# Performance work log

Hardware: AMD Instinct MI355X
Metric: run time of the kernel (lower is better)

## Reference

```python
import jax, jax.numpy as jnp
import numpy as np

DROPOUT_P = 0.5


def normalize_adj(A):
    # A_tilda = A + I ; A_hat = D^-0.5 A_tilda D^-0.5
    # The torch code does this with diag_embed + two bmm (O(N^3));
    # mathematically it is row/col broadcasting (O(N^2)).
    B, N, _ = A.shape
    A_tilda = A + jnp.eye(N, dtype=A.dtype)
    d_inv_sqrt = jnp.sum(A_tilda, axis=2) ** -0.5          # [B, N]
    return d_inv_sqrt[:, :, None] * A_tilda * d_inv_sqrt[:, None, :]


def gcn_layer(X, A_hat, W, b):
    # standard Kipf GCN layer: A_hat @ (X @ W) + b
    return jnp.einsum('bnm,bmd->bnd', A_hat, X @ W) + b


def setup_inputs() -> dict:
    key = jax.random.key(0)
    ks = jax.random.split(key, 6)
    B, N, Din, H, C = 8, 2048, 64, 64, 16
    X = jax.random.normal(ks[0], (B, N, Din), dtype=jnp.float32)
    A = jax.random.uniform(ks[1], (B, N, N), dtype=jnp.float32)
    W1 = jax.random.normal(ks[2], (Din, H), dtype=jnp.float32) * (1.0 / np.sqrt(Din))
    b1 = jax.random.normal(ks[3], (H,), dtype=jnp.float32) * 0.01
    W2 = jax.random.normal(ks[4], (H, C), dtype=jnp.float32) * (1.0 / np.sqrt(H))
    b2 = jax.random.normal(ks[5], (C,), dtype=jnp.float32) * 0.01
    return {"X": X, "A": A, "W1": W1, "b1": b1, "W2": W2, "b2": b2}


def reference(X, A, W1, b1, W2, b2):
    A_hat = normalize_adj(A)
    h = jax.nn.relu(gcn_layer(X, A_hat, W1, b1))
    # F.dropout default training=True -> apply dropout with a fixed key
    keep = jax.random.bernoulli(jax.random.key(42), 1.0 - DROPOUT_P, h.shape)
    h = jnp.where(keep, h / (1.0 - DROPOUT_P), 0.0).astype(h.dtype)
    return gcn_layer(h, A_hat, W2, b2)
```

## Files before the change

### kernel.cpp

```cpp
#include <hip/hip_runtime.h>

#define BN 16384
#define NN 2048
#define DD 64
#define CC 16

typedef short bf16x8 __attribute__((ext_vector_type(8)));
typedef float f32x4 __attribute__((ext_vector_type(4)));
typedef unsigned short u16x4 __attribute__((ext_vector_type(4)));

__device__ __forceinline__ f32x4 mfma16(bf16x8 a, bf16x8 b, f32x4 c) {
  return __builtin_amdgcn_mfma_f32_16x16x32_bf16(a, b, c, 0, 0, 0);
}
__device__ __forceinline__ unsigned short f2bf(float f) {
  unsigned u = __float_as_uint(f);
  return (unsigned short)((u + 0x7FFFu + ((u >> 16) & 1u)) >> 16);
}
__device__ __forceinline__ float bf2f(unsigned short h) {
  return __uint_as_float(((unsigned)h) << 16);
}

__device__ __forceinline__ unsigned tf_bits(unsigned i) {
  unsigned x0 = 0u;
  unsigned x1 = i;
  const unsigned k0 = 0u, k1 = 42u, k2 = 0x1BD11BDAu ^ 0u ^ 42u;
  x0 += k0; x1 += k1;
#define TFR(r) { x0 += x1; x1 = (x1 << (r)) | (x1 >> (32 - (r))); x1 ^= x0; }
  TFR(13) TFR(15) TFR(26) TFR(6)
  x0 += k1; x1 += k2 + 1u;
  TFR(17) TFR(29) TFR(16) TFR(24)
  x0 += k2; x1 += k0 + 2u;
  TFR(13) TFR(15) TFR(26) TFR(6)
  x0 += k0; x1 += k1 + 3u;
  TFR(17) TFR(29) TFR(16) TFR(24)
  x0 += k1; x1 += k2 + 4u;
  TFR(13) TFR(15) TFR(26) TFR(6)
  x0 += k2; x1 += k0 + 5u;
#undef TFR
  return x0 ^ x1;
}


__global__ __launch_bounds__(256) void k_deg(const float* __restrict__ A,
    const float* __restrict__ X, const float* __restrict__ W1,
    float* __restrict__ dis, unsigned short* __restrict__ Abf,
    unsigned short* __restrict__ Y1s, unsigned short* __restrict__ Y1sT)
{
  const int w = threadIdx.x >> 6, lane = threadIdx.x & 63;
  const size_t row = (size_t)blockIdx.x * 4 + w;
  const float4* Arow = (const float4*)(A + row * NN);
  unsigned short* Brow = Abf + row * NN;
  float s = 0.f;
#pragma unroll
  for (int it = 0; it < 8; ++it) {
    float4 v = Arow[lane + 64 * it];
    s += (v.x + v.y) + (v.z + v.w);
    u16x4 p = { f2bf(v.x), f2bf(v.y), f2bf(v.z), f2bf(v.w) };
    *(u16x4*)(Brow + lane * 4 + it * 256) = p;
  }
#pragma unroll
  for (int m = 32; m; m >>= 1) s += __shfl_xor(s, m, 64);
  const float dv = 1.0f / sqrtf(s + 1.0f);
  if (lane == 0) dis[row] = dv;
  const float* Xr = X + row * DD;
  float acc = 0.f;
#pragma unroll
  for (int k = 0; k < DD; ++k) acc += Xr[k] * W1[k * DD + lane];
  const unsigned short yv = f2bf(dv * acc);
  Y1s[row * DD + lane] = yv;
  const int b = (int)(row >> 11), kr = (int)(row & (NN - 1));
  Y1sT[((size_t)b * DD + lane) * NN + kr] = yv;
}

__global__ __launch_bounds__(256, 4) void k_gemm1h(const unsigned short* __restrict__ Abf,
    const unsigned short* __restrict__ Y1sT, const unsigned short* __restrict__ Y1s,
    const float* __restrict__ dis, const float* __restrict__ b1,
    unsigned short* __restrict__ Hbf)
{
  __shared__ float red[4][32][36];
  const int Mb = blockIdx.x >> 1;
  const int ns = blockIdx.x & 1;
  const int w = __builtin_amdgcn_readfirstlane((int)threadIdx.x >> 6);
  const int lane = threadIdx.x & 63;
  const int m15 = lane & 15, quad = lane >> 4;
  const int b = Mb >> 6;
  const int k0 = w * 512 + quad * 8;
  const unsigned short* Ap0 = Abf + ((size_t)Mb * 32 + m15) * NN + k0;
  const unsigned short* Ap1 = Ap0 + (size_t)16 * NN;
  const unsigned short* Bp0 = Y1sT + ((size_t)b * DD + ns * 32 + m15) * NN + k0;
  const unsigned short* Bp1 = Bp0 + (size_t)16 * NN;
  const f32x4 zero = 0.f;
  f32x4 acc[2][2];
  acc[0][0] = zero; acc[0][1] = zero; acc[1][0] = zero; acc[1][1] = zero;
  bf16x8 a0 = *(const bf16x8*)Ap0, a1 = *(const bf16x8*)Ap1;
  bf16x8 b0 = *(const bf16x8*)Bp0, b1v = *(const bf16x8*)Bp1;
#pragma unroll 1
  for (int kk = 0; kk < 16; ++kk) {
    const int off = (kk < 15) ? (kk + 1) * 32 : 0;
    bf16x8 na0 = *(const bf16x8*)(Ap0 + off);
    bf16x8 na1 = *(const bf16x8*)(Ap1 + off);
    bf16x8 nb0 = *(const bf16x8*)(Bp0 + off);
    bf16x8 nb1 = *(const bf16x8*)(Bp1 + off);
    acc[0][0] = mfma16(a0, b0, acc[0][0]);
    acc[0][1] = mfma16(a0, b1v, acc[0][1]);
    acc[1][0] = mfma16(a1, b0, acc[1][0]);
    acc[1][1] = mfma16(a1, b1v, acc[1][1]);
    a0 = na0; a1 = na1; b0 = nb0; b1v = nb1;
  }
#pragma unroll
  for (int mi = 0; mi < 2; ++mi)
#pragma unroll
    for (int ni = 0; ni < 2; ++ni)
#pragma unroll
      for (int r = 0; r < 4; ++r)
        red[w][mi * 16 + quad * 4 + r][ni * 16 + m15] = acc[mi][ni][r];
  __syncthreads();
  const int tid = threadIdx.x;
  const int rowl = tid >> 3, c0 = (tid & 7) * 4;
  f32x4 sum = *(const f32x4*)&red[0][rowl][c0];
  sum += *(const f32x4*)&red[1][rowl][c0];
  sum += *(const f32x4*)&red[2][rowl][c0];
  sum += *(const f32x4*)&red[3][rowl][c0];
  const int grow = Mb * 32 + rowl;
  const int gcol0 = ns * 32 + c0;
  const u16x4 y1d = *(const u16x4*)(Y1s + (size_t)grow * DD + gcol0);
  const float4 b1q = *(const float4*)(b1 + gcol0);
  const float dv = dis[grow];
  const unsigned o0 = (unsigned)grow * DD + gcol0;
  u16x4 hq;
#pragma unroll
  for (int j = 0; j < 4; ++j) {
    const float z = sum[j] + bf2f(y1d[j]);
    const float bj = j == 0 ? b1q.x : j == 1 ? b1q.y : j == 2 ? b1q.z : b1q.w;
    float h = fmaxf(dv * z + bj, 0.f);
    const unsigned bits = tf_bits(o0 + j);
    hq[j] = (bits >> 31) ? (unsigned short)0 : f2bf(h + h);
  }
  *(u16x4*)(Hbf + (size_t)grow * DD + gcol0) = hq;
}

__global__ __launch_bounds__(256) void k_epi1(const unsigned short* __restrict__ Hbf,
    const float* __restrict__ dis, const float* __restrict__ W2,
    unsigned short* __restrict__ Y2sT, float* __restrict__ S2d)
{
  __shared__ float hs[16][68];
  __shared__ float W2l[DD * CC];
  const int tid = threadIdx.x;
  *(float4*)(W2l + tid * 4) = *(const float4*)(W2 + tid * 4);
  const int r0 = blockIdx.x * 16;
  {
    const int rl = tid >> 4, cl = (tid & 15) * 4;
    const u16x4 hv = *(const u16x4*)(Hbf + ((size_t)r0 + rl) * DD + cl);
    hs[rl][cl + 0] = bf2f(hv[0]);
    hs[rl][cl + 1] = bf2f(hv[1]);
    hs[rl][cl + 2] = bf2f(hv[2]);
    hs[rl][cl + 3] = bf2f(hv[3]);
  }
  __syncthreads();
  const int c = tid & 15, rl = tid >> 4;
  float s = 0.f;
#pragma unroll
  for (int k = 0; k < DD; ++k) s += hs[rl][k] * W2l[k * CC + c];
  const int row = r0 + rl;
  const int b = row >> 11, kr = row & (NN - 1);
  const float y2 = dis[row] * s;
  Y2sT[((size_t)b * CC + c) * NN + kr] = f2bf(y2);
  S2d[(size_t)row * CC + c] = y2;
}

__global__ __launch_bounds__(256, 4) void k_gemm2o(const unsigned short* __restrict__ Abf,
    const unsigned short* __restrict__ Y2sT, const float* __restrict__ S2d,
    const float* __restrict__ dis, const float* __restrict__ b2,
    float* __restrict__ out)
{
  __shared__ float red[4][16][20];
  const int Mb = blockIdx.x;
  const int w = __builtin_amdgcn_readfirstlane((int)threadIdx.x >> 6);
  const int lane = threadIdx.x & 63;
  const int m15 = lane & 15, quad = lane >> 4;
  const int b = Mb >> 7;
  const int k0 = w * 512 + quad * 8;
  const unsigned short* Ap = Abf + ((size_t)Mb * 16 + m15) * NN + k0;
  const unsigned short* Bp = Y2sT + ((size_t)b * CC + m15) * NN + k0;
  const f32x4 zero = 0.f;
  f32x4 acc = zero;
  bf16x8 a = *(const bf16x8*)Ap;
  bf16x8 bb = *(const bf16x8*)Bp;
#pragma unroll 1
  for (int kk = 0; kk < 16; ++kk) {
    const int off = (kk < 15) ? (kk + 1) * 32 : 0;
    bf16x8 na = *(const bf16x8*)(Ap + off);
    bf16x8 nbb = *(const bf16x8*)(Bp + off);
    acc = mfma16(a, bb, acc);
    a = na; bb = nbb;
  }
#pragma unroll
  for (int r = 0; r < 4; ++r)
    red[w][quad * 4 + r][m15] = acc[r];
  __syncthreads();
  const int tid = threadIdx.x;
  const int rowl = tid >> 4, c = tid & 15;
  const float sum = red[0][rowl][c] + red[1][rowl][c]
                  + red[2][rowl][c] + red[3][rowl][c];
  const int grow = Mb * 16 + rowl;
  out[(size_t)grow * CC + c] =
      dis[grow] * (sum + S2d[(size_t)grow * CC + c]) + b2[c];
}

#define FKS1 4
#define FKS2 16

__global__ __launch_bounds__(256) void d_deg_xw(const float* __restrict__ A,
    const float* __restrict__ X, const float* __restrict__ W1,
    float* __restrict__ dis, float* __restrict__ Y1s)
{
  const int w = threadIdx.x >> 6, lane = threadIdx.x & 63;
  const int row = __builtin_amdgcn_readfirstlane(blockIdx.x * 4 + w);
  const float4* Arow = (const float4*)(A + (size_t)row * NN);
  float s = 0.f;
#pragma unroll
  for (int it = 0; it < 8; ++it) {
    float4 v = Arow[lane + 64 * it];
    s += v.x + v.y + v.z + v.w;
  }
#pragma unroll
  for (int m = 32; m; m >>= 1) s += __shfl_xor(s, m, 64);
  const float dv = 1.0f / sqrtf(s + 1.0f);
  if (lane == 0) dis[row] = dv;
  const float* Xr = X + (size_t)row * DD;
  float acc = 0.f;
#pragma unroll
  for (int k = 0; k < DD; ++k) acc += Xr[k] * W1[k * DD + lane];
  Y1s[(size_t)row * DD + lane] = dv * acc;
}

__global__ __launch_bounds__(256) void d_gemm1(const float* __restrict__ A,
    const float* __restrict__ Y1s, float* __restrict__ Z1)
{
  const int rb = blockIdx.x >> 2, ks = blockIdx.x & (FKS1 - 1);
  const int lane = threadIdx.x & 63;
  const int c0 = __builtin_amdgcn_readfirstlane((threadIdx.x >> 6) << 4);
  const int row = rb * 64 + lane;
  const int batch = rb >> 5;
  const int KSEG = NN / FKS1;
  const float* Arow = A + (size_t)row * NN + ks * KSEG;
  const float* Yb = Y1s + (size_t)batch * NN * DD + c0;
  const int kbase = ks * KSEG;
  float acc[16];
#pragma unroll
  for (int c = 0; c < 16; ++c) acc[c] = 0.f;
  float4 a0 = *(const float4*)(Arow);
  float4 a1 = *(const float4*)(Arow + 4);
  float4 a2 = *(const float4*)(Arow + 8);
  float4 a3 = *(const float4*)(Arow + 12);
  for (int k = 0; k < KSEG; k += 16) {
    const int kn = (k + 16 < KSEG) ? (k + 16) : 0;
    float4 n0 = *(const float4*)(Arow + kn);
    float4 n1 = *(const float4*)(Arow + kn + 4);
    float4 n2 = *(const float4*)(Arow + kn + 8);
    float4 n3 = *(const float4*)(Arow + kn + 12);
    const float* y0 = Yb + (size_t)(kbase + k) * DD;
    const float av[16] = {a0.x, a0.y, a0.z, a0.w, a1.x, a1.y, a1.z, a1.w,
                          a2.x, a2.y, a2.z, a2.w, a3.x, a3.y, a3.z, a3.w};
#pragma unroll
    for (int j = 0; j < 16; ++j) {
      const float* yr = y0 + j * DD;
#pragma unroll
      for (int c = 0; c < 16; ++c) acc[c] += av[j] * yr[c];
    }
    a0 = n0; a1 = n1; a2 = n2; a3 = n3;
  }
  float* Zp = Z1 + ((size_t)ks * BN + row) * DD + c0;
#pragma unroll
  for (int c = 0; c < 16; c += 4) {
    float4 v; v.x = acc[c]; v.y = acc[c+1]; v.z = acc[c+2]; v.w = acc[c+3];
    *(float4*)(Zp + c) = v;
  }
}

__global__ __launch_bounds__(256) void d_epi1(const float* __restrict__ Z1,
    const float* __restrict__ Y1s, const float* __restrict__ dis,
    const float* __restrict__ b1, const float* __restrict__ W2,
    float* __restrict__ Y2s)
{
  __shared__ float W2l[DD * CC];
  __shared__ float hl[4][DD];
  const int tid = threadIdx.x;
  *(float4*)(W2l + tid * 4) = *(const float4*)(W2 + tid * 4);
  const int w = tid >> 6, lane = tid & 63;
  const int row = blockIdx.x * 4 + w;
  const size_t o = (size_t)row * DD + lane;
  float z = Y1s[o];
#pragma unroll
  for (int p = 0; p < FKS1; ++p) z += Z1[(size_t)p * BN * DD + o];
  const float dv = dis[row];
  float h = fmaxf(dv * z + b1[lane], 0.f);
  const unsigned bits = tf_bits((unsigned)o);
  h = (bits >> 31) ? 0.f : (h + h);
  hl[w][lane] = h;
  __syncthreads();
  const int wr = tid >> 6, l = tid & 63;
  const int c = l & 15, kq = l >> 4;
  float p = 0.f;
#pragma unroll
  for (int kk = 0; kk < 16; ++kk)
    p += hl[wr][kq * 16 + kk] * W2l[(kq * 16 + kk) * CC + c];
  p += __shfl_xor(p, 16, 64);
  p += __shfl_xor(p, 32, 64);
  if (l < 16) {
    const int rg = blockIdx.x * 4 + wr;
    Y2s[(size_t)rg * CC + c] = dis[rg] * p;
  }
}

__global__ __launch_bounds__(256) void d_gemm2(const float* __restrict__ A,
    const float* __restrict__ Y2s, float* __restrict__ Z2)
{
  const int rb = blockIdx.x >> 4, ks = blockIdx.x & (FKS2 - 1);
  const int row = rb * 256 + threadIdx.x;
  const int batch = rb >> 3;
  const int KSEG = NN / FKS2;
  const float* Arow = A + (size_t)row * NN + ks * KSEG;
  const float* Yb = Y2s + (size_t)batch * NN * CC;
  const int kbase = ks * KSEG;
  float acc[16];
#pragma unroll
  for (int c = 0; c < 16; ++c) acc[c] = 0.f;
  float4 a0 = *(const float4*)(Arow);
  float4 a1 = *(const float4*)(Arow + 4);
  for (int k = 0; k < KSEG; k += 8) {
    const int kn = (k + 8 < KSEG) ? (k + 8) : 0;
    float4 n0 = *(const float4*)(Arow + kn);
    float4 n1 = *(const float4*)(Arow + kn + 4);
    const float av[8] = {a0.x, a0.y, a0.z, a0.w, a1.x, a1.y, a1.z, a1.w};
#pragma unroll
    for (int j = 0; j < 8; ++j) {
      const float* yr = Yb + (size_t)(kbase + k + j) * CC;
#pragma unroll
      for (int c = 0; c < 16; ++c) acc[c] += av[j] * yr[c];
    }
    a0 = n0; a1 = n1;
  }
  float* Zp = Z2 + ((size_t)ks * BN + row) * CC;
#pragma unroll
  for (int c = 0; c < 16; c += 4) {
    float4 v; v.x = acc[c]; v.y = acc[c+1]; v.z = acc[c+2]; v.w = acc[c+3];
    *(float4*)(Zp + c) = v;
  }
}

__global__ __launch_bounds__(256) void d_final(const float* __restrict__ Z2,
    const float* __restrict__ Y2s, const float* __restrict__ dis,
    const float* __restrict__ b2, float* __restrict__ out)
{
  const int gid = blockIdx.x * 256 + threadIdx.x;
  const int r = gid >> 2, q = gid & 3;
  const size_t o = (size_t)r * CC + q * 4;
  float4 s = *(const float4*)(Y2s + o);
#pragma unroll
  for (int p = 0; p < FKS2; ++p) {
    const float4 zp = *(const float4*)(Z2 + (size_t)p * BN * CC + o);
    s.x += zp.x; s.y += zp.y; s.z += zp.z; s.w += zp.w;
  }
  const float dv = dis[r];
  const float4 bb = *(const float4*)(b2 + q * 4);
  float4 res;
  res.x = dv * s.x + bb.x;
  res.y = dv * s.y + bb.y;
  res.z = dv * s.z + bb.z;
  res.w = dv * s.w + bb.w;
  *(float4*)(out + o) = res;
}

extern "C" void kernel_launch(void* const* d_in, const int* in_sizes, int n_in,
                              void* d_out, int out_size, void* d_ws, size_t ws_size,
                              hipStream_t stream) {
  const float* X  = (const float*)d_in[0];
  const float* A  = (const float*)d_in[1];
  const float* W1 = (const float*)d_in[2];
  const float* b1 = (const float*)d_in[3];
  const float* W2 = (const float*)d_in[4];
  const float* b2 = (const float*)d_in[5];
  float* out = (float*)d_out;
  char* wsb = (char*)d_ws;

  const size_t NEED = 75038720;
  if (ws_size >= NEED) {
    unsigned short* Abf  = (unsigned short*)wsb;
    unsigned short* Y1s  = (unsigned short*)(wsb + 67108864);
    unsigned short* Y1sT = (unsigned short*)(wsb + 69206016);
    unsigned short* Hbf  = (unsigned short*)(wsb + 71303168);
    unsigned short* Y2sT = (unsigned short*)(wsb + 73400320);
    float*          S2d  = (float*)(wsb + 73924608);
    float*          dis  = (float*)(wsb + 74973184);

    k_deg   <<<BN / 4, 256, 0, stream>>>(A, X, W1, dis, Abf, Y1s, Y1sT);
    k_gemm1h<<<1024,   256, 0, stream>>>(Abf, Y1sT, Y1s, dis, b1, Hbf);
    k_epi1  <<<1024,   256, 0, stream>>>(Hbf, dis, W2, Y2sT, S2d);
    k_gemm2o<<<1024,   256, 0, stream>>>(Abf, Y2sT, S2d, dis, b2, out);
  } else {
    float* ws  = (float*)d_ws;
    float* dis = ws;
    float* Y1s = ws + 16384;
    float* Z1  = Y1s + (size_t)BN * DD;
    float* Z2  = Z1;
    float* Y2s = Z1 + (size_t)FKS1 * BN * DD;

    d_deg_xw<<<BN / 4,     256, 0, stream>>>(A, X, W1, dis, Y1s);
    d_gemm1 <<<256 * FKS1, 256, 0, stream>>>(A, Y1s, Z1);
    d_epi1  <<<BN / 4,     256, 0, stream>>>(Z1, Y1s, dis, b1, W2, Y2s);
    d_gemm2 <<<64 * FKS2,  256, 0, stream>>>(A, Y2s, Z2);
    d_final <<<256,        256, 0, stream>>>(Z2, Y2s, dis, b2, out);
  }
}
```

Before: 271.2 us.

## Fuse layer-1 epilogue into gemm1 with full-width row tiles

The first adjacency GEMM now computes all 64 hidden columns per 16-row block instead of splitting the columns across two blocks. This lets the ReLU/dropout output stay in shared memory and be multiplied by W2 in the same kernel. The separate epilogue kernel and the global bf16 H buffer are removed, and each A row tile is read once instead of twice. Each block now does more MFMA work per A load and needs more LDS, with fewer blocks in flight per row.

```diff
diff --git a/kernel.cpp b/kernel.cpp
--- a/kernel.cpp
+++ b/kernel.cpp
@@ -72,100 +72,84 @@
   Y1sT[((size_t)b * DD + lane) * NN + kr] = yv;
 }
 
-__global__ __launch_bounds__(256, 4) void k_gemm1h(const unsigned short* __restrict__ Abf,
+__global__ __launch_bounds__(256, 4) void k_gemm1f(const unsigned short* __restrict__ Abf,
     const unsigned short* __restrict__ Y1sT, const unsigned short* __restrict__ Y1s,
     const float* __restrict__ dis, const float* __restrict__ b1,
-    unsigned short* __restrict__ Hbf)
-{
-  __shared__ float red[4][32][36];
-  const int Mb = blockIdx.x >> 1;
-  const int ns = blockIdx.x & 1;
-  const int w = __builtin_amdgcn_readfirstlane((int)threadIdx.x >> 6);
-  const int lane = threadIdx.x & 63;
+    const float* __restrict__ W2,
+    unsigned short* __restrict__ Y2sT, float* __restrict__ S2d)
+{
+  __shared__ float red[4][16][68];
+  __shared__ float W2l[DD * CC];
+  const int tid = threadIdx.x;
+  *(float4*)(W2l + tid * 4) = *(const float4*)(W2 + tid * 4);
+  const int Mb = blockIdx.x;
+  const int w = __builtin_amdgcn_readfirstlane((int)tid >> 6);
+  const int lane = tid & 63;
   const int m15 = lane & 15, quad = lane >> 4;
-  const int b = Mb >> 6;
+  const int b = Mb >> 7;
   const int k0 = w * 512 + quad * 8;
-  const unsigned short* Ap0 = Abf + ((size_t)Mb * 32 + m15) * NN + k0;
-  const unsigned short* Ap1 = Ap0 + (size_t)16 * NN;
-  const unsigned short* Bp0 = Y1sT + ((size_t)b * DD + ns * 32 + m15) * NN + k0;
+  const unsigned short* Ap  = Abf + ((size_t)Mb * 16 + m15) * NN + k0;
+  const unsigned short* Bp0 = Y1sT + ((size_t)b * DD + m15) * NN + k0;
   const unsigned short* Bp1 = Bp0 + (size_t)16 * NN;
+  const unsigned short* Bp2 = Bp0 + (size_t)32 * NN;
+  const unsigned short* Bp3 = Bp0 + (size_t)48 * NN;
   const f32x4 zero = 0.f;
-  f32x4 acc[2][2];
-  acc[0][0] = zero; acc[0][1] = zero; acc[1][0] = zero; acc[1][1] = zero;
-  bf16x8 a0 = *(const bf16x8*)Ap0, a1 = *(const bf16x8*)Ap1;
+  f32x4 acc[4];
+  acc[0] = zero; acc[1] = zero; acc[2] = zero; acc[3] = zero;
+  bf16x8 a  = *(const bf16x8*)Ap;
   bf16x8 b0 = *(const bf16x8*)Bp0, b1v = *(const bf16x8*)Bp1;
+  bf16x8 b2v = *(const bf16x8*)Bp2, b3v = *(const bf16x8*)Bp3;
 #pragma unroll 1
   for (int kk = 0; kk < 16; ++kk) {
     const int off = (kk < 15) ? (kk + 1) * 32 : 0;
-    bf16x8 na0 = *(const bf16x8*)(Ap0 + off);
-    bf16x8 na1 = *(const bf16x8*)(Ap1 + off);
+    bf16x8 na  = *(const bf16x8*)(Ap + off);
     bf16x8 nb0 = *(const bf16x8*)(Bp0 + off);
     bf16x8 nb1 = *(const bf16x8*)(Bp1 + off);
-    acc[0][0] = mfma16(a0, b0, acc[0][0]);
-    acc[0][1] = mfma16(a0, b1v, acc[0][1]);
-    acc[1][0] = mfma16(a1, b0, acc[1][0]);
-    acc[1][1] = mfma16(a1, b1v, acc[1][1]);
-    a0 = na0; a1 = na1; b0 = nb0; b1v = nb1;
-  }
-#pragma unroll
-  for (int mi = 0; mi < 2; ++mi)
-#pragma unroll
-    for (int ni = 0; ni < 2; ++ni)
-#pragma unroll
-      for (int r = 0; r < 4; ++r)
-        red[w][mi * 16 + quad * 4 + r][ni * 16 + m15] = acc[mi][ni][r];
-  __syncthreads();
-  const int tid = threadIdx.x;
-  const int rowl = tid >> 3, c0 = (tid & 7) * 4;
+    bf16x8 nb2 = *(const bf16x8*)(Bp2 + off);
+    bf16x8 nb3 = *(const bf16x8*)(Bp3 + off);
+    acc[0] = mfma16(a, b0,  acc[0]);
+    acc[1] = mfma16(a, b1v, acc[1]);
+    acc[2] = mfma16(a, b2v, acc[2]);
+    acc[3] = mfma16(a, b3v, acc[3]);
+    a = na; b0 = nb0; b1v = nb1; b2v = nb2; b3v = nb3;
+  }
+#pragma unroll
+  for (int ni = 0; ni < 4; ++ni)
+#pragma unroll
+    for (int r = 0; r < 4; ++r)
+      red[w][quad * 4 + r][ni * 16 + m15] = acc[ni][r];
+  __syncthreads();
+  const int rowl = tid >> 4, c0 = (tid & 15) * 4;
   f32x4 sum = *(const f32x4*)&red[0][rowl][c0];
   sum += *(const f32x4*)&red[1][rowl][c0];
   sum += *(const f32x4*)&red[2][rowl][c0];
   sum += *(const f32x4*)&red[3][rowl][c0];
-  const int grow = Mb * 32 + rowl;
-  const int gcol0 = ns * 32 + c0;
-  const u16x4 y1d = *(const u16x4*)(Y1s + (size_t)grow * DD + gcol0);
-  const float4 b1q = *(const float4*)(b1 + gcol0);
+  const int grow = Mb * 16 + rowl;
+  const u16x4 y1d = *(const u16x4*)(Y1s + (size_t)grow * DD + c0);
+  const float4 b1q = *(const float4*)(b1 + c0);
   const float dv = dis[grow];
-  const unsigned o0 = (unsigned)grow * DD + gcol0;
-  u16x4 hq;
+  const unsigned o0 = (unsigned)grow * DD + c0;
+  f32x4 hq;
 #pragma unroll
   for (int j = 0; j < 4; ++j) {
     const float z = sum[j] + bf2f(y1d[j]);
     const float bj = j == 0 ? b1q.x : j == 1 ? b1q.y : j == 2 ? b1q.z : b1q.w;
     float h = fmaxf(dv * z + bj, 0.f);
     const unsigned bits = tf_bits(o0 + j);
-    hq[j] = (bits >> 31) ? (unsigned short)0 : f2bf(h + h);
-  }
-  *(u16x4*)(Hbf + (size_t)grow * DD + gcol0) = hq;
-}
-
-__global__ __launch_bounds__(256) void k_epi1(const unsigned short* __restrict__ Hbf,
-    const float* __restrict__ dis, const float* __restrict__ W2,
-    unsigned short* __restrict__ Y2sT, float* __restrict__ S2d)
-{
-  __shared__ float hs[16][68];
-  __shared__ float W2l[DD * CC];
-  const int tid = threadIdx.x;
-  *(float4*)(W2l + tid * 4) = *(const float4*)(W2 + tid * 4);
-  const int r0 = blockIdx.x * 16;
-  {
-    const int rl = tid >> 4, cl = (tid & 15) * 4;
-    const u16x4 hv = *(const u16x4*)(Hbf + ((size_t)r0 + rl) * DD + cl);
-    hs[rl][cl + 0] = bf2f(hv[0]);
-    hs[rl][cl + 1] = bf2f(hv[1]);
-    hs[rl][cl + 2] = bf2f(hv[2]);
-    hs[rl][cl + 3] = bf2f(hv[3]);
-  }
-  __syncthreads();
-  const int c = tid & 15, rl = tid >> 4;
+    hq[j] = (bits >> 31) ? 0.f : (h + h);
+  }
+  __syncthreads();
+  *(f32x4*)&red[0][rowl][c0] = hq;
+  __syncthreads();
+  const float* hrow = &red[0][rowl][0];
+  const int c2 = tid & 15;
   float s = 0.f;
 #pragma unroll
-  for (int k = 0; k < DD; ++k) s += hs[rl][k] * W2l[k * CC + c];
-  const int row = r0 + rl;
-  const int b = row >> 11, kr = row & (NN - 1);
-  const float y2 = dis[row] * s;
-  Y2sT[((size_t)b * CC + c) * NN + kr] = f2bf(y2);
-  S2d[(size_t)row * CC + c] = y2;
+  for (int k = 0; k < DD; ++k) s += hrow[k] * W2l[k * CC + c2];
+  const float y2 = dv * s;
+  S2d[(size_t)grow * CC + c2] = y2;
+  const int kr = grow & (NN - 1);
+  Y2sT[((size_t)b * CC + c2) * NN + kr] = f2bf(y2);
 }
 
 __global__ __launch_bounds__(256, 4) void k_gemm2o(const unsigned short* __restrict__ Abf,
@@ -384,20 +368,18 @@
   float* out = (float*)d_out;
   char* wsb = (char*)d_ws;
 
-  const size_t NEED = 75038720;
+  const size_t NEED = 72941568;
   if (ws_size >= NEED) {
     unsigned short* Abf  = (unsigned short*)wsb;
     unsigned short* Y1s  = (unsigned short*)(wsb + 67108864);
     unsigned short* Y1sT = (unsigned short*)(wsb + 69206016);
-    unsigned short* Hbf  = (unsigned short*)(wsb + 71303168);
-    unsigned short* Y2sT = (unsigned short*)(wsb + 73400320);
-    float*          S2d  = (float*)(wsb + 73924608);
-    float*          dis  = (float*)(wsb + 74973184);
-
-    k_deg   <<<BN / 4, 256, 0, stream>>>(A, X, W1, dis, Abf, Y1s, Y1sT);
-    k_gemm1h<<<1024,   256, 0, stream>>>(Abf, Y1sT, Y1s, dis, b1, Hbf);
-    k_epi1  <<<1024,   256, 0, stream>>>(Hbf, dis, W2, Y2sT, S2d);
-    k_gemm2o<<<1024,   256, 0, stream>>>(Abf, Y2sT, S2d, dis, b2, out);
+    unsigned short* Y2sT = (unsigned short*)(wsb + 71303168);
+    float*          S2d  = (float*)(wsb + 71827456);
+    float*          dis  = (float*)(wsb + 72876032);
+
+    k_deg   <<<BN / 4,  256, 0, stream>>>(A, X, W1, dis, Abf, Y1s, Y1sT);
+    k_gemm1f<<<BN / 16, 256, 0, stream>>>(Abf, Y1sT, Y1s, dis, b1, W2, Y2sT, S2d);
+    k_gemm2o<<<1024,    256, 0, stream>>>(Abf, Y2sT, S2d, dis, b2, out);
   } else {
     float* ws  = (float*)d_ws;
     float* dis = ws;
```

Result: no change. 270.5 us (-0.3%).
